# Optimization experiments

Measured on AMD Instinct MI355X. Metric: run time of the kernel, lower is better.

## Reference

```python
import jax, jax.numpy as jnp
import numpy as np

K = 1024  # codebook size
D = 256   # embedding dim


def setup_inputs() -> dict:
    key = jax.random.key(0)
    k1, k2 = jax.random.split(key)
    z_e_x = jax.random.normal(k1, (32, D, 32, 32), dtype=jnp.float32)  # NCHW
    # nn.Embedding weight initialized uniform(-1/K, 1/K)
    W = jax.random.uniform(k2, (K, D), dtype=jnp.float32, minval=-1.0 / K, maxval=1.0 / K)
    return {"z_e_x": z_e_x, "W": W}


def reference(z_e_x, W):
    # permute NCHW -> NHWC, flatten spatial, nearest-codebook lookup (vq)
    z = jnp.transpose(z_e_x, (0, 2, 3, 1))            # [B, H, Wd, D]
    B, H, Wd, Dd = z.shape
    flat = z.reshape(-1, Dd)                           # [N, D]
    # squared L2 distances: ||z||^2 - 2 z.W^T + ||W||^2
    z_sq = jnp.sum(flat * flat, axis=1, keepdims=True)         # [N, 1]
    w_sq = jnp.sum(W * W, axis=1)                               # [K]
    dists = z_sq - 2.0 * (flat @ W.T) + w_sq[None, :]           # [N, K]
    idx = jnp.argmin(dists, axis=1)                             # [N]
    latents = idx.reshape(B, H, Wd)                             # [B, H, Wd] int indices
    return latents
```

## Files before the change

### kernel.cpp

```cpp
#include <hip/hip_runtime.h>

#define NPOS 32768
#define DDIM 256
#define KCODES 1024

typedef __attribute__((ext_vector_type(8))) short bf16x8;
typedef __attribute__((ext_vector_type(4))) float f32x4;
typedef unsigned long long u64;

__device__ __forceinline__ float sqr_rn(float x) {
    float r = x * x;
    asm volatile("" : "+v"(r));
    return r;
}
__device__ __forceinline__ float add_rn(float a, float b) {
    float r = a + b;
    asm volatile("" : "+v"(r));
    return r;
}

__device__ __forceinline__ unsigned short f2bf(float x) {
    unsigned u = __float_as_uint(x);
    return (unsigned short)((u + 0x7fffu + ((u >> 16) & 1u)) >> 16);
}

__device__ __forceinline__ u64 packm(float s, int code) {
    unsigned b = __float_as_uint(s);
    unsigned mm = ((unsigned)((int)b >> 31)) | 0x80000000u;
    return ((u64)(b ^ mm) << 32) | (unsigned)code;
}

__global__ __launch_bounds__(256) void wprep(const float* __restrict__ W,
                                             float* __restrict__ wsq,
                                             unsigned short* __restrict__ wb16t) {
    const int t   = threadIdx.x;
    const int bid = blockIdx.x;
    const int row = bid * 16 + (t >> 4);
    const int j   = t & 15;
    const float* base = W + row * DDIM + (j & 7) + (j >> 3) * 128;
    float r = sqr_rn(base[0]);
#pragma unroll
    for (int i = 1; i < 16; ++i) r = add_rn(r, sqr_rn(base[i * 8]));
#pragma unroll
    for (int m = 1; m <= 8; m <<= 1) r = add_rn(r, __shfl_xor(r, m));
    if (j == 0) wsq[row] = r;
#pragma unroll
    for (int jj = 0; jj < 2; ++jj) {
        const int u  = t + jj * 256;
        const int n  = bid * 16 + (u >> 5);
        const int k8 = u & 31;
        const float4 f0 = *(const float4*)&W[n * DDIM + k8 * 8];
        const float4 f1 = *(const float4*)&W[n * DDIM + k8 * 8 + 4];
        bf16x8 o;
        o[0] = (short)f2bf(f0.x); o[1] = (short)f2bf(f0.y);
        o[2] = (short)f2bf(f0.z); o[3] = (short)f2bf(f0.w);
        o[4] = (short)f2bf(f1.x); o[5] = (short)f2bf(f1.y);
        o[6] = (short)f2bf(f1.z); o[7] = (short)f2bf(f1.w);
        const int kk = k8 >> 2, kq = k8 & 3;
        *(bf16x8*)&wb16t[(n >> 8) * 65536 + kk * 8192 + kq * 2048 + (n & 255) * 8] = o;
    }
}

#define ZS 260
__global__ __launch_bounds__(256) __attribute__((amdgpu_waves_per_eu(2, 2)))
void vq_fused(const float* __restrict__ z,
              const float* __restrict__ W,
              const float* __restrict__ wsq,
              const unsigned short* __restrict__ wb16t,
              int* __restrict__ out) {
    union Sm {
        unsigned short At[16384];
        float          Zs[32 * ZS];
    };
    __shared__ Sm  sm;
    __shared__ u64 redL[64 * 8];
    __shared__ u64 candL[64 * 8];

    const int t   = threadIdx.x;
    const int bid = blockIdx.x;
    const int img = bid >> 4;
    const int p0  = (bid & 15) * 64;

    {
        const float* zbase = z + img * (DDIM * 1024) + p0;
#pragma unroll
        for (int jj = 0; jj < 8; ++jj) {
            const int u_ = t + jj * 256;
            const int m  = u_ & 63;
            const int k8 = u_ >> 6;
            const float* src = zbase + k8 * 8192 + m;
            bf16x8 o;
#pragma unroll
            for (int e = 0; e < 8; ++e) o[e] = (short)f2bf(src[e * 1024]);
            *(bf16x8*)&sm.At[k8 * 512 + m * 8] = o;
        }
    }
    __syncthreads();

    const int w  = t >> 6;
    const int l  = t & 63;
    const int ln = l & 15;
    const int q  = l >> 4;
    const int nw = w * 64;

    const char* aBase = (const char*)sm.At + q * 1024 + ln * 16;
    const char* bBase = (const char*)wb16t + q * 4096 + (nw + ln) * 16;

#pragma unroll 1
    for (int nblk = 0; nblk < 4; ++nblk) {
        const int n0 = nblk * 256;
        float wq[4];
#pragma unroll
        for (int nf = 0; nf < 4; ++nf) wq[nf] = wsq[n0 + nw + nf * 16 + ln];

        f32x4 acc[4][4];
#pragma unroll
        for (int a = 0; a < 4; ++a)
#pragma unroll
            for (int b = 0; b < 4; ++b) acc[a][b] = (f32x4)(0.f);

        const char* bP = bBase + nblk * 131072;
        bf16x8 bfr[4], bnx[4];
#pragma unroll
        for (int nf = 0; nf < 4; ++nf) bfr[nf] = *(const bf16x8*)(bP + nf * 256);

#pragma unroll 1
        for (int kk = 0; kk < 8; ++kk) {
            if (kk < 7) {
#pragma unroll
                for (int nf = 0; nf < 4; ++nf)
                    bnx[nf] = *(const bf16x8*)(bP + (kk + 1) * 16384 + nf * 256);
            }
            bf16x8 afr[4];
#pragma unroll
            for (int mf = 0; mf < 4; ++mf)
                afr[mf] = *(const bf16x8*)(aBase + kk * 4096 + mf * 256);
#pragma unroll
            for (int nf = 0; nf < 4; ++nf)
#pragma unroll
                for (int mf = 0; mf < 4; ++mf)
                    acc[mf][nf] = __builtin_amdgcn_mfma_f32_16x16x32_bf16(
                        afr[mf], bfr[nf], acc[mf][nf], 0, 0, 0);
#pragma unroll
            for (int nf = 0; nf < 4; ++nf) bfr[nf] = bnx[nf];
        }

#pragma unroll
        for (int mf = 0; mf < 4; ++mf) {
#pragma unroll
            for (int reg = 0; reg < 4; ++reg) {
                const int row = mf * 16 + q * 4 + reg;
                float s0 = 1e30f, s1 = 1e30f;
                int   i0 = 0,     i1 = 0;
#pragma unroll
                for (int nf = 0; nf < 4; ++nf) {
                    const float s  = fmaf(-2.f, acc[mf][nf][reg], wq[nf]);
                    const int   cc = n0 + nw + nf * 16 + ln;
                    if (s < s0)      { s1 = s0; i1 = i0; s0 = s; i0 = cc; }
                    else if (s < s1) { s1 = s; i1 = cc; }
                }
                u64 c0 = packm(s0, i0), c1 = packm(s1, i1);
#pragma unroll
                for (int m = 1; m <= 8; m <<= 1) {
                    const u64 o0 = __shfl_xor(c0, m);
                    const u64 o1 = __shfl_xor(c1, m);
                    const u64 hi = (c0 < o0) ? o0 : c0;
                    c0 = (c0 < o0) ? c0 : o0;
                    const u64 lo = (c1 < o1) ? c1 : o1;
                    c1 = (hi < lo) ? hi : lo;
                }
                if (ln == 0) {
                    redL[row * 8 + w * 2]     = c0;
                    redL[row * 8 + w * 2 + 1] = c1;
                }
            }
        }
        __syncthreads();
        if (t < 64) {
            u64 c0 = ~0ull, c1 = ~0ull;
#pragma unroll
            for (int jj = 0; jj < 8; ++jj) {
                const u64 v = redL[t * 8 + jj];
                if (v < c0)      { c1 = c0; c0 = v; }
                else if (v < c1) { c1 = v; }
            }
            candL[t * 8 + nblk * 2]     = c0;
            candL[t * 8 + nblk * 2 + 1] = c1;
        }
        __syncthreads();
    }

    const float* zimg = z + img * (DDIM * 1024) + p0;
#pragma unroll 1
    for (int c = 0; c < 2; ++c) {
#pragma unroll
        for (int jj = 0; jj < 8; ++jj) {
            const int f4 = t + jj * 256;
            const int d = f4 >> 3, p4 = f4 & 7;
            const float4 v = *(const float4*)&zimg[d * 1024 + c * 32 + p4 * 4];
            sm.Zs[(p4 * 4 + 0) * ZS + d] = v.x;
            sm.Zs[(p4 * 4 + 1) * ZS + d] = v.y;
            sm.Zs[(p4 * 4 + 2) * ZS + d] = v.z;
            sm.Zs[(p4 * 4 + 3) * ZS + d] = v.w;
        }
        __syncthreads();
        const int pl = t >> 3, slot = t & 7;
        const float* zr = &sm.Zs[pl * ZS];

        float h0 = sqr_rn(zr[slot]);
        float h1 = sqr_rn(zr[128 + slot]);
#pragma unroll
        for (int i = 1; i < 16; ++i) {
            h0 = add_rn(h0, sqr_rn(zr[slot + 8 * i]));
            h1 = add_rn(h1, sqr_rn(zr[128 + slot + 8 * i]));
        }
#pragma unroll
        for (int m = 1; m <= 4; m <<= 1) {
            h0 = add_rn(h0, __shfl_xor(h0, m));
            h1 = add_rn(h1, __shfl_xor(h1, m));
        }
        const float zq = add_rn(h0, h1);

        const int code = (int)(unsigned)(candL[(c * 32 + pl) * 8 + slot] & 0xffffffffULL);
        const float* wr = W + code * DDIM;
        float M = 0.f;
#pragma unroll 8
        for (int d4 = 0; d4 < 64; ++d4) {
            const float4 zv = *(const float4*)&zr[d4 * 4];
            const float4 wv = *(const float4*)&wr[d4 * 4];
            M = fmaf(zv.x, wv.x, M);
            M = fmaf(zv.y, wv.y, M);
            M = fmaf(zv.z, wv.z, M);
            M = fmaf(zv.w, wv.w, M);
        }
        const float s = add_rn(fmaf(-2.f, M, zq), wsq[code]);
        u64 v = ((u64)__float_as_uint(s) << 32) | (unsigned)code;
#pragma unroll
        for (int m = 1; m <= 4; m <<= 1) {
            const u64 o = __shfl_xor(v, m);
            if (o < v) v = o;
        }
        if (slot == 0) out[img * 1024 + p0 + c * 32 + pl] = (int)(unsigned)(v & 0xffffffffULL);
        __syncthreads();
    }
}

extern "C" void kernel_launch(void* const* d_in, const int* in_sizes, int n_in,
                              void* d_out, int out_size, void* d_ws, size_t ws_size,
                              hipStream_t stream) {
    const float* z = (const float*)d_in[0];
    const float* W = (const float*)d_in[1];
    int* out = (int*)d_out;

    char* ws = (char*)d_ws;
    float*          wsq   = (float*)ws;
    unsigned short* wb16t = (unsigned short*)(ws + 4096);

    wprep<<<KCODES / 16, 256, 0, stream>>>(W, wsq, wb16t);
    vq_fused<<<NPOS / 64, 256, 0, stream>>>(z, W, wsq, wb16t, out);
}
```

Before: 152.4 us.

## Retile MFMA warps to 32x128 with double-buffered B fragments

New measurement: 143.8 us. -5.6%, faster.

```diff
diff --git a/kernel.cpp b/kernel.cpp
--- a/kernel.cpp
+++ b/kernel.cpp
@@ -62,7 +62,7 @@
 }
 
 #define ZS 260
-__global__ __launch_bounds__(256) __attribute__((amdgpu_waves_per_eu(2, 2)))
+__global__ __launch_bounds__(256)
 void vq_fused(const float* __restrict__ z,
               const float* __restrict__ W,
               const float* __restrict__ wsq,
@@ -73,7 +73,7 @@
         float          Zs[32 * ZS];
     };
     __shared__ Sm  sm;
-    __shared__ u64 redL[64 * 8];
+    __shared__ u64 redP[64 * 4];
     __shared__ u64 candL[64 * 8];
 
     const int t   = threadIdx.x;
@@ -101,59 +101,77 @@
     const int l  = t & 63;
     const int ln = l & 15;
     const int q  = l >> 4;
-    const int nw = w * 64;
-
-    const char* aBase = (const char*)sm.At + q * 1024 + ln * 16;
+    const int mw = (w & 1) * 32;
+    const int nh = w >> 1;
+    const int nw = nh * 128;
+
+    const char* aBase = (const char*)sm.At + q * 1024 + (mw + ln) * 16;
     const char* bBase = (const char*)wb16t + q * 4096 + (nw + ln) * 16;
 
 #pragma unroll 1
     for (int nblk = 0; nblk < 4; ++nblk) {
         const int n0 = nblk * 256;
-        float wq[4];
-#pragma unroll
-        for (int nf = 0; nf < 4; ++nf) wq[nf] = wsq[n0 + nw + nf * 16 + ln];
-
-        f32x4 acc[4][4];
-#pragma unroll
-        for (int a = 0; a < 4; ++a)
-#pragma unroll
-            for (int b = 0; b < 4; ++b) acc[a][b] = (f32x4)(0.f);
+        float wq[8];
+#pragma unroll
+        for (int nf = 0; nf < 8; ++nf) wq[nf] = wsq[n0 + nw + nf * 16 + ln];
+
+        f32x4 acc[2][8];
+#pragma unroll
+        for (int a = 0; a < 2; ++a)
+#pragma unroll
+            for (int b = 0; b < 8; ++b) acc[a][b] = (f32x4)(0.f);
 
         const char* bP = bBase + nblk * 131072;
-        bf16x8 bfr[4], bnx[4];
-#pragma unroll
-        for (int nf = 0; nf < 4; ++nf) bfr[nf] = *(const bf16x8*)(bP + nf * 256);
+        bf16x8 bA[8], bB[8];
+#pragma unroll
+        for (int nf = 0; nf < 8; ++nf) bA[nf] = *(const bf16x8*)(bP + nf * 256);
 
 #pragma unroll 1
-        for (int kk = 0; kk < 8; ++kk) {
-            if (kk < 7) {
-#pragma unroll
-                for (int nf = 0; nf < 4; ++nf)
-                    bnx[nf] = *(const bf16x8*)(bP + (kk + 1) * 16384 + nf * 256);
-            }
-            bf16x8 afr[4];
-#pragma unroll
-            for (int mf = 0; mf < 4; ++mf)
-                afr[mf] = *(const bf16x8*)(aBase + kk * 4096 + mf * 256);
-#pragma unroll
-            for (int nf = 0; nf < 4; ++nf)
-#pragma unroll
-                for (int mf = 0; mf < 4; ++mf)
-                    acc[mf][nf] = __builtin_amdgcn_mfma_f32_16x16x32_bf16(
-                        afr[mf], bfr[nf], acc[mf][nf], 0, 0, 0);
-#pragma unroll
-            for (int nf = 0; nf < 4; ++nf) bfr[nf] = bnx[nf];
-        }
-
-#pragma unroll
-        for (int mf = 0; mf < 4; ++mf) {
+        for (int kk2 = 0; kk2 < 4; ++kk2) {
+            const int kkE = kk2 * 2;
+#pragma unroll
+            for (int nf = 0; nf < 8; ++nf)
+                bB[nf] = *(const bf16x8*)(bP + (kkE + 1) * 16384 + nf * 256);
+            {
+                bf16x8 afr[2];
+#pragma unroll
+                for (int mf = 0; mf < 2; ++mf)
+                    afr[mf] = *(const bf16x8*)(aBase + kkE * 4096 + mf * 256);
+#pragma unroll
+                for (int nf = 0; nf < 8; ++nf)
+#pragma unroll
+                    for (int mf = 0; mf < 2; ++mf)
+                        acc[mf][nf] = __builtin_amdgcn_mfma_f32_16x16x32_bf16(
+                            afr[mf], bA[nf], acc[mf][nf], 0, 0, 0);
+            }
+            if (kk2 < 3) {
+#pragma unroll
+                for (int nf = 0; nf < 8; ++nf)
+                    bA[nf] = *(const bf16x8*)(bP + (kkE + 2) * 16384 + nf * 256);
+            }
+            {
+                bf16x8 afr[2];
+#pragma unroll
+                for (int mf = 0; mf < 2; ++mf)
+                    afr[mf] = *(const bf16x8*)(aBase + (kkE + 1) * 4096 + mf * 256);
+#pragma unroll
+                for (int nf = 0; nf < 8; ++nf)
+#pragma unroll
+                    for (int mf = 0; mf < 2; ++mf)
+                        acc[mf][nf] = __builtin_amdgcn_mfma_f32_16x16x32_bf16(
+                            afr[mf], bB[nf], acc[mf][nf], 0, 0, 0);
+            }
+        }
+
+#pragma unroll
+        for (int mf = 0; mf < 2; ++mf) {
 #pragma unroll
             for (int reg = 0; reg < 4; ++reg) {
-                const int row = mf * 16 + q * 4 + reg;
+                const int row = mw + mf * 16 + q * 4 + reg;
                 float s0 = 1e30f, s1 = 1e30f;
                 int   i0 = 0,     i1 = 0;
 #pragma unroll
-                for (int nf = 0; nf < 4; ++nf) {
+                for (int nf = 0; nf < 8; ++nf) {
                     const float s  = fmaf(-2.f, acc[mf][nf][reg], wq[nf]);
                     const int   cc = n0 + nw + nf * 16 + ln;
                     if (s < s0)      { s1 = s0; i1 = i0; s0 = s; i0 = cc; }
@@ -170,77 +188,78 @@
                     c1 = (hi < lo) ? hi : lo;
                 }
                 if (ln == 0) {
-                    redL[row * 8 + w * 2]     = c0;
-                    redL[row * 8 + w * 2 + 1] = c1;
+                    redP[row * 4 + nh * 2]     = c0;
+                    redP[row * 4 + nh * 2 + 1] = c1;
                 }
             }
         }
         __syncthreads();
         if (t < 64) {
-            u64 c0 = ~0ull, c1 = ~0ull;
-#pragma unroll
-            for (int jj = 0; jj < 8; ++jj) {
-                const u64 v = redL[t * 8 + jj];
-                if (v < c0)      { c1 = c0; c0 = v; }
-                else if (v < c1) { c1 = v; }
-            }
-            candL[t * 8 + nblk * 2]     = c0;
-            candL[t * 8 + nblk * 2 + 1] = c1;
+            const u64 a = redP[t * 4],     b = redP[t * 4 + 1];
+            const u64 c = redP[t * 4 + 2], d = redP[t * 4 + 3];
+            const u64 m1 = (a < c) ? a : c;
+            const u64 hi = (a < c) ? c : a;
+            const u64 lo = (b < d) ? b : d;
+            const u64 m2 = (hi < lo) ? hi : lo;
+            candL[t * 8 + nblk * 2]     = m1;
+            candL[t * 8 + nblk * 2 + 1] = m2;
         }
         __syncthreads();
     }
 
     const float* zimg = z + img * (DDIM * 1024) + p0;
 #pragma unroll 1
-    for (int c = 0; c < 2; ++c) {
+    for (int ch = 0; ch < 2; ++ch) {
 #pragma unroll
         for (int jj = 0; jj < 8; ++jj) {
             const int f4 = t + jj * 256;
             const int d = f4 >> 3, p4 = f4 & 7;
-            const float4 v = *(const float4*)&zimg[d * 1024 + c * 32 + p4 * 4];
+            const float4 v = *(const float4*)&zimg[d * 1024 + ch * 32 + p4 * 4];
             sm.Zs[(p4 * 4 + 0) * ZS + d] = v.x;
             sm.Zs[(p4 * 4 + 1) * ZS + d] = v.y;
             sm.Zs[(p4 * 4 + 2) * ZS + d] = v.z;
             sm.Zs[(p4 * 4 + 3) * ZS + d] = v.w;
         }
         __syncthreads();
-        const int pl = t >> 3, slot = t & 7;
-        const float* zr = &sm.Zs[pl * ZS];
-
-        float h0 = sqr_rn(zr[slot]);
-        float h1 = sqr_rn(zr[128 + slot]);
-#pragma unroll
-        for (int i = 1; i < 16; ++i) {
-            h0 = add_rn(h0, sqr_rn(zr[slot + 8 * i]));
-            h1 = add_rn(h1, sqr_rn(zr[128 + slot + 8 * i]));
-        }
-#pragma unroll
-        for (int m = 1; m <= 4; m <<= 1) {
-            h0 = add_rn(h0, __shfl_xor(h0, m));
-            h1 = add_rn(h1, __shfl_xor(h1, m));
-        }
-        const float zq = add_rn(h0, h1);
-
-        const int code = (int)(unsigned)(candL[(c * 32 + pl) * 8 + slot] & 0xffffffffULL);
-        const float* wr = W + code * DDIM;
-        float M = 0.f;
+        {
+            const int pl = t >> 3, slot = t & 7;
+            const float* zr = &sm.Zs[pl * ZS];
+
+            float h0 = sqr_rn(zr[slot]);
+            float h1 = sqr_rn(zr[128 + slot]);
+#pragma unroll
+            for (int i = 1; i < 16; ++i) {
+                h0 = add_rn(h0, sqr_rn(zr[slot + 8 * i]));
+                h1 = add_rn(h1, sqr_rn(zr[128 + slot + 8 * i]));
+            }
+#pragma unroll
+            for (int m = 1; m <= 4; m <<= 1) {
+                h0 = add_rn(h0, __shfl_xor(h0, m));
+                h1 = add_rn(h1, __shfl_xor(h1, m));
+            }
+            const float zq = add_rn(h0, h1);
+
+            const int code = (int)(unsigned)(candL[(ch * 32 + pl) * 8 + slot] & 0xffffffffULL);
+            const float* wr = W + code * DDIM;
+            float M = 0.f;
 #pragma unroll 8
-        for (int d4 = 0; d4 < 64; ++d4) {
-            const float4 zv = *(const float4*)&zr[d4 * 4];
-            const float4 wv = *(const float4*)&wr[d4 * 4];
-            M = fmaf(zv.x, wv.x, M);
-            M = fmaf(zv.y, wv.y, M);
-            M = fmaf(zv.z, wv.z, M);
-            M = fmaf(zv.w, wv.w, M);
-        }
-        const float s = add_rn(fmaf(-2.f, M, zq), wsq[code]);
-        u64 v = ((u64)__float_as_uint(s) << 32) | (unsigned)code;
-#pragma unroll
-        for (int m = 1; m <= 4; m <<= 1) {
-            const u64 o = __shfl_xor(v, m);
-            if (o < v) v = o;
-        }
-        if (slot == 0) out[img * 1024 + p0 + c * 32 + pl] = (int)(unsigned)(v & 0xffffffffULL);
+            for (int d4 = 0; d4 < 64; ++d4) {
+                const float4 zv = *(const float4*)&zr[d4 * 4];
+                const float4 wv = *(const float4*)&wr[d4 * 4];
+                M = fmaf(zv.x, wv.x, M);
+                M = fmaf(zv.y, wv.y, M);
+                M = fmaf(zv.z, wv.z, M);
+                M = fmaf(zv.w, wv.w, M);
+            }
+            const float s = add_rn(fmaf(-2.f, M, zq), wsq[code]);
+            u64 v = ((u64)__float_as_uint(s) << 32) | (unsigned)code;
+#pragma unroll
+            for (int m = 1; m <= 4; m <<= 1) {
+                const u64 o = __shfl_xor(v, m);
+                if (o < v) v = o;
+            }
+            if (slot == 0) out[img * 1024 + p0 + ch * 32 + pl] = (int)(unsigned)(v & 0xffffffffULL);
+        }
         __syncthreads();
     }
 }
```
